# Performance work log

Measured on AMD Instinct MI355X. Metric: run time of the kernel, lower is better.

## Reference

```python
import jax, jax.numpy as jnp
import numpy as np

N, E = 50000, 800000
IN_C, H_C, OUT_C, HEADS = 64, 32, 32, 8


def setup_inputs() -> dict:
    key = jax.random.key(0)
    ks = jax.random.split(key, 16)
    def glorot(k, shape):
        fan_in = shape[-1]
        return jax.random.normal(k, shape, dtype=jnp.float32) / jnp.sqrt(jnp.float32(fan_in))
    inp = {
        'x': jax.random.normal(ks[0], (N, IN_C), dtype=jnp.float32),
        'edge_index': jax.random.randint(ks[1], (2, E), 0, N, dtype=jnp.int64),
        # layer 1: in_c -> h_c, heads
        'W1l': glorot(ks[2], (HEADS * H_C, IN_C)),
        'b1l': jnp.zeros((HEADS * H_C,), jnp.float32),
        'W1r': glorot(ks[3], (HEADS * H_C, IN_C)),
        'b1r': jnp.zeros((HEADS * H_C,), jnp.float32),
        'att1': glorot(ks[4], (HEADS, H_C)),
        'bias1': jnp.zeros((H_C,), jnp.float32),
        # layer 2: h_c -> out_c, heads
        'W2l': glorot(ks[5], (HEADS * OUT_C, H_C)),
        'b2l': jnp.zeros((HEADS * OUT_C,), jnp.float32),
        'W2r': glorot(ks[6], (HEADS * OUT_C, H_C)),
        'b2r': jnp.zeros((HEADS * OUT_C,), jnp.float32),
        'att2': glorot(ks[7], (HEADS, OUT_C)),
        'bias2': jnp.zeros((OUT_C,), jnp.float32),
    }
    return inp


def _gatv2_layer(x, src, dst, valid, Wl, bl, Wr, br, att, bias):
    # PyG GATv2Conv (share_weights=False, concat=False): message j->i uses
    # e = att . leaky_relu(lin_l(x_j) + lin_r(x_i), 0.2); softmax over dst; agg lin_l(x_j).
    n = x.shape[0]
    heads, c = att.shape
    xl = (x @ Wl.T + bl).reshape(n, heads, c)
    xr = (x @ Wr.T + br).reshape(n, heads, c)
    m = jax.nn.leaky_relu(xl[src] + xr[dst], negative_slope=0.2)  # [Etot,H,C]
    score = jnp.einsum('ehc,hc->eh', m, att)                      # [Etot,H]
    score = jnp.where(valid[:, None], score, -jnp.inf)
    smax = jax.ops.segment_max(score, dst, num_segments=n)        # [N,H]
    a = jnp.where(valid[:, None], jnp.exp(score - smax[dst]), 0.0)
    denom = jax.ops.segment_sum(a, dst, num_segments=n)
    a = a / jnp.maximum(denom[dst], 1e-16)
    out = jax.ops.segment_sum(a[..., None] * xl[src], dst, num_segments=n)  # [N,H,C]
    return out.mean(axis=1) + bias


def reference(x, edge_index, W1l, b1l, W1r, b1r, att1, bias1,
              W2l, b2l, W2r, b2r, att2, bias2):
    n = x.shape[0]
    src0, dst0 = edge_index[0], edge_index[1]
    # PyG removes existing self loops then adds fresh ones: mask originals,
    # append one self loop per node (keeps static shapes).
    loop = jnp.arange(n, dtype=src0.dtype)
    src = jnp.concatenate([src0, loop])
    dst = jnp.concatenate([dst0, loop])
    valid = jnp.concatenate([src0 != dst0, jnp.ones((n,), bool)])
    h = _gatv2_layer(x, src, dst, valid, W1l, b1l, W1r, b1r, att1, bias1)
    h = jax.nn.leaky_relu(h, negative_slope=0.01)  # nn.LeakyReLU default
    out = _gatv2_layer(h, src, dst, valid, W2l, b2l, W2r, b2r, att2, bias2)
    return out
```

## Files before the change

### kernel.cpp

```cpp
#include <hip/hip_runtime.h>
#include <math.h>

#define HEADS 8
#define CDIM 32
#define ODIM 256

typedef _Float16 h2 __attribute__((ext_vector_type(2)));
typedef _Float16 h4 __attribute__((ext_vector_type(4)));
union H4 { h4 v; h2 p[2]; };

#if __has_builtin(__builtin_amdgcn_fdot2)
#define FDOT2(a,b,c) __builtin_amdgcn_fdot2((a),(b),(c),false)
#else
static __device__ __forceinline__ float fdot2_sw(h2 a, h2 b, float c){
  return fmaf((float)a.x, (float)b.x, fmaf((float)a.y, (float)b.y, c));
}
#define FDOT2(a,b,c) fdot2_sw((a),(b),(c))
#endif

__device__ __forceinline__ float lrelu(float v, float s){ return fmaxf(v, s*v); }

__global__ void block_sum_kernel(const int* __restrict__ counts, int* __restrict__ bsums, int n){
  int i = blockIdx.x*256 + threadIdx.x;
  int v = (i < n) ? counts[i] : 0;
#pragma unroll
  for (int off=1; off<64; off<<=1) v += __shfl_xor(v, off);
  __shared__ int ws[4];
  int lane = threadIdx.x & 63, w = threadIdx.x >> 6;
  if (lane == 0) ws[w] = v;
  __syncthreads();
  if (threadIdx.x == 0) bsums[blockIdx.x] = ws[0]+ws[1]+ws[2]+ws[3];
}

__global__ __launch_bounds__(1024) void scan_bsums_kernel(int* __restrict__ bsums, int nb){
  __shared__ int s[1024];
  int t = threadIdx.x;
  int v = (t < nb) ? bsums[t] : 0;
  s[t] = v;
  __syncthreads();
  for (int off=1; off<1024; off<<=1){
    int u = (t >= off) ? s[t-off] : 0;
    __syncthreads();
    s[t] += u;
    __syncthreads();
  }
  if (t < nb) bsums[t] = s[t] - v;
}

__global__ void local_scan_kernel(const int* __restrict__ counts, const int* __restrict__ bsums,
                                  int* __restrict__ indptr, int n){
  __shared__ int s[256];
  int t = threadIdx.x;
  int i = blockIdx.x*256 + t;
  int v = (i < n) ? counts[i] : 0;
  s[t] = v;
  __syncthreads();
  for (int off=1; off<256; off<<=1){
    int u = (t >= off) ? s[t-off] : 0;
    __syncthreads();
    s[t] += u;
    __syncthreads();
  }
  int excl = s[t] - v + bsums[blockIdx.x];
  if (i < n) indptr[i] = excl;
  if (i == n-1) indptr[n] = excl + v;
}

__global__ void scatter_kernel(const int* __restrict__ src, const int* __restrict__ dst,
                               const int* __restrict__ rank, const int* __restrict__ indptr,
                               int* __restrict__ csr_src, int e){
  int i = blockIdx.x*256 + threadIdx.x;
  if (i < e){
    int r = rank[i];
    if (r >= 0){
      int d = dst[i];
      csr_src[indptr[d] + r] = src[i];
    }
  }
}

template<int K, bool FUSE_COUNT>
__global__ __launch_bounds__(256, 2) void gemm_kernel(const float* __restrict__ X,
    const float* __restrict__ Wl, const float* __restrict__ bl,
    const float* __restrict__ Wr, const float* __restrict__ br,
    _Float16* __restrict__ outl, _Float16* __restrict__ outr, int n,
    const int* __restrict__ src, const int* __restrict__ dst,
    int* __restrict__ counts, int* __restrict__ rank, int e){
  if (FUSE_COUNT && blockIdx.y == 0){
    const int CB = 96;
    if (blockIdx.x < CB){
      int stride = CB*256;
      for (int i = blockIdx.x*256 + threadIdx.x; i < e; i += stride){
        int s = src[i], d = dst[i];
        int r = -1;
        if (s != d) r = atomicAdd(counts + d, 1);
        rank[i] = r;
      }
    }
    return;
  }
  const int KP = K + 4;
  __shared__ float xt[128*(K+4)];
  __shared__ float wt[2][64*(K+4)];
  int t = threadIdx.x;
  int n0 = blockIdx.x*128;
  int o0 = (FUSE_COUNT ? (blockIdx.y-1) : blockIdx.y)*64;

  for (int idx = t; idx < 128*(K/4); idx += 256){
    int row = idx/(K/4), c = (idx%(K/4))*4;
    int node = n0 + row; if (node >= n) node = n-1;
    *(float4*)(xt + row*KP + c) = *(const float4*)(X + (size_t)node*K + c);
  }
  for (int idx = t; idx < 64*(K/4); idx += 256){
    int row = idx/(K/4), c = (idx%(K/4))*4;
    *(float4*)(wt[0] + row*KP + c) = *(const float4*)(Wl + (size_t)(o0+row)*K + c);
    *(float4*)(wt[1] + row*KP + c) = *(const float4*)(Wr + (size_t)(o0+row)*K + c);
  }
  __syncthreads();

  int og = t & 15;
  int ng = t >> 4;
  float accl[8][4] = {{0.f}}, accr[8][4] = {{0.f}};

#pragma unroll 2
  for (int kk = 0; kk < K; kk += 4){
    float4 xv[8], wl4[4], wr4[4];
#pragma unroll
    for (int i=0;i<8;i++) xv[i] = *(const float4*)(xt + (ng+16*i)*KP + kk);
#pragma unroll
    for (int j=0;j<4;j++){
      wl4[j] = *(const float4*)(wt[0] + (og+16*j)*KP + kk);
      wr4[j] = *(const float4*)(wt[1] + (og+16*j)*KP + kk);
    }
#pragma unroll
    for (int i=0;i<8;i++){
#pragma unroll
      for (int j=0;j<4;j++){
        accl[i][j] = fmaf(xv[i].x, wl4[j].x, fmaf(xv[i].y, wl4[j].y,
                     fmaf(xv[i].z, wl4[j].z, fmaf(xv[i].w, wl4[j].w, accl[i][j]))));
        accr[i][j] = fmaf(xv[i].x, wr4[j].x, fmaf(xv[i].y, wr4[j].y,
                     fmaf(xv[i].z, wr4[j].z, fmaf(xv[i].w, wr4[j].w, accr[i][j]))));
      }
    }
  }

  float bvl[4], bvr[4];
#pragma unroll
  for (int j=0;j<4;j++){ bvl[j] = bl[o0+og+16*j]; bvr[j] = br[o0+og+16*j]; }
#pragma unroll
  for (int i=0;i<8;i++){
    int node = n0 + ng + 16*i;
    if (node < n){
      _Float16* pl = outl + (size_t)node*ODIM + o0 + og;
      _Float16* pr = outr + (size_t)node*ODIM + o0 + og;
#pragma unroll
      for (int j=0;j<4;j++){
        pl[16*j] = (_Float16)(accl[i][j] + bvl[j]);
        pr[16*j] = (_Float16)(accr[i][j] + bvr[j]);
      }
    }
  }
}

__global__ __launch_bounds__(256) void edge_kernel(
    const _Float16* __restrict__ xl, const _Float16* __restrict__ xr,
    const float* __restrict__ att, const float* __restrict__ bias,
    const int* __restrict__ indptr, const int* __restrict__ csr_src,
    float* __restrict__ out, int n, int act)
{
  int wid = blockIdx.x*4 + (threadIdx.x >> 6);
  if (wid >= n) return;
  int lane = threadIdx.x & 63;
  const float LOG2E = 1.44269504088896341f;

  float4 attf = *(const float4*)(att + 4*lane);
  h2 at0 = (h2){(_Float16)(attf.x*LOG2E), (_Float16)(attf.y*LOG2E)};
  h2 at1 = (h2){(_Float16)(attf.z*LOG2E), (_Float16)(attf.w*LOG2E)};
  const h2 c02 = {(_Float16)0.2f, (_Float16)0.2f};

  H4 xrh; xrh.v = *(const h4*)(xr + (size_t)wid*ODIM + 4*lane);
  H4 self; self.v = *(const h4*)(xl + (size_t)wid*ODIM + 4*lane);

  auto score = [&](const H4& c)->float{
    h2 t0 = c.p[0] + xrh.p[0];
    h2 t1 = c.p[1] + xrh.p[1];
    h2 q0 = __builtin_elementwise_max(t0, t0 * c02);
    h2 q1 = __builtin_elementwise_max(t1, t1 * c02);
    float d = FDOT2(q0, at0, FDOT2(q1, at1, 0.f));
    d += __shfl_xor(d, 1);
    d += __shfl_xor(d, 2);
    d += __shfl_xor(d, 4);
    return d;
  };

  float w0 = exp2f(score(self));
  float denom = w0;
  float4 acc;
  acc.x = w0 * (float)self.v.x;
  acc.y = w0 * (float)self.v.y;
  acc.z = w0 * (float)self.v.z;
  acc.w = w0 * (float)self.v.w;

  int beg = __builtin_amdgcn_readfirstlane(indptr[wid]);
  int end = __builtin_amdgcn_readfirstlane(indptr[wid+1]);
  int cnt = end - beg;
  H4 r0, r1;
  r0.v = (h4){}; r1.v = (h4){};
  if (cnt > 0){
    int s0 = __builtin_amdgcn_readfirstlane(csr_src[beg]);
    r0.v = *(const h4*)(xl + (size_t)s0*ODIM + 4*lane);
  }
  if (cnt > 1){
    int s1 = __builtin_amdgcn_readfirstlane(csr_src[beg+1]);
    r1.v = *(const h4*)(xl + (size_t)s1*ODIM + 4*lane);
  }
  for (int k = 0; k < cnt; ++k){
    H4 cur = r0; r0 = r1;
    if (k+2 < cnt){
      int s2 = __builtin_amdgcn_readfirstlane(csr_src[beg+k+2]);
      r1.v = *(const h4*)(xl + (size_t)s2*ODIM + 4*lane);
    }
    float pe = exp2f(score(cur));
    denom += pe;
    acc.x = fmaf(pe, (float)cur.v.x, acc.x);
    acc.y = fmaf(pe, (float)cur.v.y, acc.y);
    acc.z = fmaf(pe, (float)cur.v.z, acc.z);
    acc.w = fmaf(pe, (float)cur.v.w, acc.w);
  }
  float inv = 1.f/denom;
  float vx = acc.x*inv, vy = acc.y*inv, vz = acc.z*inv, vw = acc.w*inv;
  vx += __shfl_xor(vx, 8);  vx += __shfl_xor(vx, 16);  vx += __shfl_xor(vx, 32);
  vy += __shfl_xor(vy, 8);  vy += __shfl_xor(vy, 16);  vy += __shfl_xor(vy, 32);
  vz += __shfl_xor(vz, 8);  vz += __shfl_xor(vz, 16);  vz += __shfl_xor(vz, 32);
  vw += __shfl_xor(vw, 8);  vw += __shfl_xor(vw, 16);  vw += __shfl_xor(vw, 32);
  if (lane < 8){
    float4 bv = *(const float4*)(bias + 4*lane);
    float ox = vx*0.125f + bv.x;
    float oy = vy*0.125f + bv.y;
    float oz = vz*0.125f + bv.z;
    float ow = vw*0.125f + bv.w;
    if (act){
      ox = lrelu(ox, 0.01f); oy = lrelu(oy, 0.01f);
      oz = lrelu(oz, 0.01f); ow = lrelu(ow, 0.01f);
    }
    *(float4*)(out + (size_t)wid*CDIM + 4*lane) = make_float4(ox, oy, oz, ow);
  }
}

extern "C" void kernel_launch(void* const* d_in, const int* in_sizes, int n_in,
                              void* d_out, int out_size, void* d_ws, size_t ws_size,
                              hipStream_t stream){
  (void)n_in; (void)out_size; (void)ws_size;
  const float* x    = (const float*)d_in[0];
  const int*   ei   = (const int*)d_in[1];
  const float* W1l  = (const float*)d_in[2];
  const float* b1l  = (const float*)d_in[3];
  const float* W1r  = (const float*)d_in[4];
  const float* b1r  = (const float*)d_in[5];
  const float* att1 = (const float*)d_in[6];
  const float* bias1= (const float*)d_in[7];
  const float* W2l  = (const float*)d_in[8];
  const float* b2l  = (const float*)d_in[9];
  const float* W2r  = (const float*)d_in[10];
  const float* b2r  = (const float*)d_in[11];
  const float* att2 = (const float*)d_in[12];
  const float* bias2= (const float*)d_in[13];
  int n = in_sizes[0] / 64;
  int e = in_sizes[1] / 2;
  const int* src = ei;
  const int* dst = ei + e;

  char* ws = (char*)d_ws;
  size_t off = 0;
  auto alloc = [&](size_t bytes)->char*{
    char* p = ws + off; off += (bytes + 255) & ~(size_t)255; return p;
  };
  _Float16* xl  = (_Float16*)alloc((size_t)n*ODIM*2);
  _Float16* xr  = (_Float16*)alloc((size_t)n*ODIM*2);
  float* h      = (float*)alloc((size_t)n*CDIM*4);
  int*   counts = (int*)alloc((size_t)n*4);
  int*   indptr = (int*)alloc((size_t)(n+1)*4);
  int*   rank   = (int*)alloc((size_t)e*4);
  int*   csr    = (int*)alloc((size_t)e*4);
  int*   bsums  = (int*)alloc((size_t)1024*4);

  int nblk = (n + 255) / 256;
  int ntiles = (n + 127) / 128;
  hipMemsetAsync(counts, 0, (size_t)n*4, stream);

  gemm_kernel<64,true><<<dim3(ntiles,5), 256, 0, stream>>>(
      x, W1l, b1l, W1r, b1r, xl, xr, n, src, dst, counts, rank, e);
  block_sum_kernel<<<nblk, 256, 0, stream>>>(counts, bsums, n);
  scan_bsums_kernel<<<1, 1024, 0, stream>>>(bsums, nblk);
  local_scan_kernel<<<nblk, 256, 0, stream>>>(counts, bsums, indptr, n);
  scatter_kernel<<<(e+255)/256, 256, 0, stream>>>(src, dst, rank, indptr, csr, e);

  edge_kernel<<<(n+3)/4, 256, 0, stream>>>(xl, xr, att1, bias1, indptr, csr, h, n, 1);
  gemm_kernel<32,false><<<dim3(ntiles,4), 256, 0, stream>>>(
      h, W2l, b2l, W2r, b2r, xl, xr, n, nullptr, nullptr, nullptr, nullptr, 0);
  edge_kernel<<<(n+3)/4, 256, 0, stream>>>(xl, xr, att2, bias2, indptr, csr, (float*)d_out, n, 0);
}
```

Measured before the change: 330.9 us.

## Fuse three-kernel prefix scan into single-pass scan with inter-block flags

Replaces the block-sum, block-sums scan, and local scan kernels with one kernel. Each block publishes its total to a flag array initialised to -1 by a new memset. Every later block spin-waits on the flags of all earlier blocks and sums them, which removes two kernel launches and their gaps. In exchange it adds one memset and relies on earlier blocks being scheduled before later ones to avoid deadlock, with redundant O(nblk) flag reads per block.

```diff
diff --git a/kernel.cpp b/kernel.cpp
--- a/kernel.cpp
+++ b/kernel.cpp
@@ -20,38 +20,14 @@
 
 __device__ __forceinline__ float lrelu(float v, float s){ return fmaxf(v, s*v); }
 
-__global__ void block_sum_kernel(const int* __restrict__ counts, int* __restrict__ bsums, int n){
-  int i = blockIdx.x*256 + threadIdx.x;
-  int v = (i < n) ? counts[i] : 0;
-#pragma unroll
-  for (int off=1; off<64; off<<=1) v += __shfl_xor(v, off);
+__global__ void scan_fused_kernel(const int* __restrict__ counts,
+                                  int* __restrict__ indptr,
+                                  int* __restrict__ flags, int n){
+  __shared__ int s[256];
   __shared__ int ws[4];
-  int lane = threadIdx.x & 63, w = threadIdx.x >> 6;
-  if (lane == 0) ws[w] = v;
-  __syncthreads();
-  if (threadIdx.x == 0) bsums[blockIdx.x] = ws[0]+ws[1]+ws[2]+ws[3];
-}
-
-__global__ __launch_bounds__(1024) void scan_bsums_kernel(int* __restrict__ bsums, int nb){
-  __shared__ int s[1024];
   int t = threadIdx.x;
-  int v = (t < nb) ? bsums[t] : 0;
-  s[t] = v;
-  __syncthreads();
-  for (int off=1; off<1024; off<<=1){
-    int u = (t >= off) ? s[t-off] : 0;
-    __syncthreads();
-    s[t] += u;
-    __syncthreads();
-  }
-  if (t < nb) bsums[t] = s[t] - v;
-}
-
-__global__ void local_scan_kernel(const int* __restrict__ counts, const int* __restrict__ bsums,
-                                  int* __restrict__ indptr, int n){
-  __shared__ int s[256];
-  int t = threadIdx.x;
-  int i = blockIdx.x*256 + t;
+  int b = blockIdx.x;
+  int i = b*256 + t;
   int v = (i < n) ? counts[i] : 0;
   s[t] = v;
   __syncthreads();
@@ -61,7 +37,19 @@
     s[t] += u;
     __syncthreads();
   }
-  int excl = s[t] - v + bsums[blockIdx.x];
+  if (t == 255) atomicExch(&flags[b], s[255]);
+  int pre = 0;
+  if (t < b){
+    int f;
+    do { f = __atomic_load_n((const int*)&flags[t], __ATOMIC_RELAXED); } while (f < 0);
+    pre = f;
+  }
+#pragma unroll
+  for (int off=1; off<64; off<<=1) pre += __shfl_xor(pre, off);
+  if ((t & 63) == 0) ws[t >> 6] = pre;
+  __syncthreads();
+  int total_prev = ws[0]+ws[1]+ws[2]+ws[3];
+  int excl = total_prev + s[t] - v;
   if (i < n) indptr[i] = excl;
   if (i == n-1) indptr[n] = excl + v;
 }
@@ -282,17 +270,16 @@
   int*   indptr = (int*)alloc((size_t)(n+1)*4);
   int*   rank   = (int*)alloc((size_t)e*4);
   int*   csr    = (int*)alloc((size_t)e*4);
-  int*   bsums  = (int*)alloc((size_t)1024*4);
+  int*   flags  = (int*)alloc((size_t)1024*4);
 
   int nblk = (n + 255) / 256;
   int ntiles = (n + 127) / 128;
-  hipMemsetAsync(counts, 0, (size_t)n*4, stream);
+  (void)hipMemsetAsync(counts, 0, (size_t)n*4, stream);
+  (void)hipMemsetAsync(flags, 0xFF, (size_t)nblk*4, stream);
 
   gemm_kernel<64,true><<<dim3(ntiles,5), 256, 0, stream>>>(
       x, W1l, b1l, W1r, b1r, xl, xr, n, src, dst, counts, rank, e);
-  block_sum_kernel<<<nblk, 256, 0, stream>>>(counts, bsums, n);
-  scan_bsums_kernel<<<1, 1024, 0, stream>>>(bsums, nblk);
-  local_scan_kernel<<<nblk, 256, 0, stream>>>(counts, bsums, indptr, n);
+  scan_fused_kernel<<<nblk, 256, 0, stream>>>(counts, indptr, flags, n);
   scatter_kernel<<<(e+255)/256, 256, 0, stream>>>(src, dst, rank, indptr, csr, e);
 
   edge_kernel<<<(n+3)/4, 256, 0, stream>>>(xl, xr, att1, bias1, indptr, csr, h, n, 1);
```

Measured after the change: 332.5 us. Within noise of the previous version (+0.5%).
